# Performance work log

Measured on AMD Instinct MI355X. Metric: run time of the kernel, lower is better.

## Reference

```python
import jax, jax.numpy as jnp
import numpy as np

NUM_QUERIES = 256
NUM_NEGATIVES = 512
NUM_GENERALIZED = 8
GEN_RADIUS = 1.0
TEMP = 0.5
STRONG_THRESHOLD = 0.97


def _mls(mu0, mu1, s0, s1):
    # mutual likelihood score; mu's are L2-normalized (F.normalize, eps=1e-12)
    mu0 = mu0 / jnp.maximum(jnp.linalg.norm(mu0, axis=-1, keepdims=True), 1e-12)
    mu1 = mu1 / jnp.maximum(jnp.linalg.norm(mu1, axis=-1, keepdims=True), 1e-12)
    down = s0 + s1
    return -0.5 * (((mu0 - mu1) ** 2) / down + jnp.log(down)).mean(-1)


def setup_inputs() -> dict:
    key = jax.random.key(0)
    B, S, H, W, C = 4, 19, 128, 128, 256
    ks = jax.random.split(key, 6)
    mu = jax.random.normal(ks[0], (B, C, H, W), jnp.float32)
    sigma = jax.random.uniform(ks[1], (B, C, H, W), jnp.float32, minval=0.1, maxval=1.0)
    cls = jax.random.randint(ks[2], (B, H, W), 0, S)
    label = jnp.transpose(jax.nn.one_hot(cls, S, dtype=jnp.float32), (0, 3, 1, 2))  # [B,S,H,W]
    mask = jnp.ones((B, 1, H, W), jnp.float32)
    prob = jax.random.uniform(ks[3], (B, S, H, W), jnp.float32)
    mmt_prototype_mu = jax.random.normal(ks[4], (S, 1, C), jnp.float32)
    mmt_prototype_sigma = jax.random.uniform(ks[5], (S, 1, C), jnp.float32, minval=0.1, maxval=1.0)
    return {"mu": mu, "sigma": sigma, "label": label, "mask": mask, "prob": prob,
            "mmt_prototype_mu": mmt_prototype_mu, "mmt_prototype_sigma": mmt_prototype_sigma,
            "epoch": 0, "iter_i": 0}


def reference(mu, sigma, label, mask, prob, mmt_prototype_mu, mmt_prototype_sigma, epoch, iter_i):
    B, C, H, W = mu.shape
    S = label.shape[1]
    P = B * H * W
    Q, NEG, G = NUM_QUERIES, NUM_NEGATIVES, NUM_GENERALIZED
    key = jax.random.key(1234)

    valid = (label * mask).transpose(1, 0, 2, 3).reshape(S, P)            # [S,P] float
    mu_f = mu.transpose(0, 2, 3, 1).reshape(P, C)                          # [P,C]
    sg_f = sigma.transpose(0, 2, 3, 1).reshape(P, C)
    prob_f = prob.transpose(1, 0, 2, 3).reshape(S, P)
    hard = (prob_f < STRONG_THRESHOLD).astype(valid.dtype) * valid         # [S,P]

    # --- segment prototypes (precision-weighted fusion), detached as in torch.no_grad ---
    inv_sg = 1.0 / sg_f
    proto_sigma_b = 1.0 / jnp.einsum('sp,pc->sc', valid, inv_sg)           # [S,C]
    proto_mu_b = proto_sigma_b * jnp.einsum('sp,pc->sc', valid, inv_sg * mu_f)
    mmt_mu = mmt_prototype_mu[:, 0, :]
    mmt_sg = mmt_prototype_sigma[:, 0, :]
    proto_sigma = 1.0 / (1.0 / proto_sigma_b + 1.0 / mmt_sg)               # momentum fusion
    proto_mu = proto_sigma * (mmt_mu / mmt_sg + proto_mu_b / proto_sigma_b)
    proto_mu = jax.lax.stop_gradient(proto_mu)
    proto_sigma = jax.lax.stop_gradient(proto_sigma)

    # cumulative masks for uniform sampling over valid / hard pixels via searchsorted
    valid_cum = jnp.cumsum(valid, axis=1)                                  # [S,P]
    valid_cnt = valid_cum[:, -1]
    hard_cum = jnp.cumsum(hard, axis=1)
    hard_cnt = hard_cum[:, -1]

    loss = jnp.float32(0.0)
    for i in range(S):
        ki = jax.random.fold_in(key, i)
        k_anc, k_cls, k_neg, k_gen = jax.random.split(ki, 4)
        # anchors: uniform over hard pixels of segment i
        u = jax.random.uniform(k_anc, (Q,)) * hard_cnt[i]
        a_idx = jnp.clip(jnp.searchsorted(hard_cum[i], u, side='right'), 0, P - 1)
        anchor_mu = mu_f[a_idx]                                            # [Q,C]
        anchor_sg = sg_f[a_idx]
        # negative class distribution from prototype MLS similarity
        others = jnp.concatenate([jnp.arange(i + 1, S), jnp.arange(0, i)])  # [S-1]
        sim = _mls(proto_mu[i][None], proto_mu[others], proto_sigma[i][None], proto_sigma[others])
        logp = jax.nn.log_softmax(sim / TEMP)
        samp = jax.random.categorical(k_cls, logp, shape=(Q, NEG))          # idx into `others`
        cls_g = others[samp.reshape(-1)]                                    # [Q*NEG] global class
        # uniform pixel within each sampled class (vectorized searchsorted over classes)
        un = jax.random.uniform(k_neg, (Q * NEG,))
        idx_all = jax.vmap(lambda cs, cnt: jnp.searchsorted(cs, un * cnt, side='right'))(valid_cum, valid_cnt)
        n_idx = jnp.clip(idx_all[cls_g, jnp.arange(Q * NEG)], 0, P - 1)
        neg_mu = jax.lax.stop_gradient(mu_f[n_idx].reshape(Q, NEG, C))
        neg_sg = jax.lax.stop_gradient(sg_f[n_idx].reshape(Q, NEG, C))
        pos_mu = jnp.broadcast_to(proto_mu[i][None, None], (Q, 1, C))
        pos_sg = jnp.broadcast_to(proto_sigma[i][None, None], (Q, 1, C))
        # generalized negatives: reparameterized samples from (updated) momentum prototypes
        eps = jax.random.normal(k_gen, (S - 1, G, C))
        gen = proto_mu[others][:, None, :] + GEN_RADIUS * jnp.sqrt(proto_sigma[others])[:, None, :] * eps
        gen = jnp.broadcast_to(gen.reshape(1, (S - 1) * G, C), (Q, (S - 1) * G, C))
        all_mu = jnp.concatenate([pos_mu, neg_mu, gen], axis=1)             # [Q,1+NEG+(S-1)*G,C]
        all_sg = jnp.concatenate([pos_sg, neg_sg, jnp.zeros_like(gen)], axis=1)
        logits = _mls(anchor_mu[:, None, :], all_mu, anchor_sg[:, None, :], all_sg) / TEMP
        loss = loss - jax.nn.log_softmax(logits, axis=-1)[:, 0].mean()      # CE vs target 0
    return loss / S
```

## Files before the change

### kernel.cpp

```cpp
#include <hip/hip_runtime.h>
#include <hip/hip_fp16.h>
#include <hip/hip_fp8.h>
#include <cstdint>

#define B_   4
#define S_   19
#define HW_  16384
#define P_   65536
#define C_   256
#define Q_   256
#define NEG_ 512
#define NS_  131072
#define GENV_ 144
#define NANCH (S_ * Q_)
#define NPAIR (NANCH / 2)
#define NBUCK 8

typedef float v2f __attribute__((ext_vector_type(2)));

#if __has_builtin(__builtin_amdgcn_cvt_pk_f32_fp8) && __has_builtin(__builtin_amdgcn_cvt_pk_fp8_f32)
#define HAVE_HW_FP8 1
#endif

template<int W> __device__ __forceinline__ v2f cvt8(uint32_t d) {
#ifdef HAVE_HW_FP8
  v2f r = __builtin_amdgcn_cvt_pk_f32_fp8((int)d, W);
  return r;
#else
  __hip_fp8_e4m3 h0, h1;
  h0.__x = (uint8_t)(d >> (W * 16));
  h1.__x = (uint8_t)(d >> (W * 16 + 8));
  v2f r; r.x = (float)h0; r.y = (float)h1; return r;
#endif
}
template<int W> __device__ __forceinline__ uint32_t pk8(float a, float b, uint32_t old) {
#ifdef HAVE_HW_FP8
  return (uint32_t)__builtin_amdgcn_cvt_pk_fp8_f32(a, b, (int)old, W);
#else
  __hip_fp8_e4m3 ha(a), hb(b);
  uint32_t v = (uint32_t)ha.__x | ((uint32_t)hb.__x << 8);
  return (old & (W ? 0x0000FFFFu : 0xFFFF0000u)) | (v << (W * 16));
#endif
}

__device__ __forceinline__ void tf2x32(uint32_t k0, uint32_t k1, uint32_t x0, uint32_t x1,
                                       uint32_t& o0, uint32_t& o1) {
  uint32_t k2 = k0 ^ k1 ^ 0x1BD11BDAu;
#define TFR(r) { x0 += x1; x1 = (x1 << r) | (x1 >> (32 - r)); x1 ^= x0; }
  x0 += k0; x1 += k1;
  TFR(13) TFR(15) TFR(26) TFR(6)  x0 += k1; x1 += k2 + 1u;
  TFR(17) TFR(29) TFR(16) TFR(24) x0 += k2; x1 += k0 + 2u;
  TFR(13) TFR(15) TFR(26) TFR(6)  x0 += k0; x1 += k1 + 3u;
  TFR(17) TFR(29) TFR(16) TFR(24) x0 += k1; x1 += k2 + 4u;
  TFR(13) TFR(15) TFR(26) TFR(6)  x0 += k2; x1 += k0 + 5u;
#undef TFR
  o0 = x0; o1 = x1;
}

__device__ __forceinline__ uint32_t rbits(uint32_t k0, uint32_t k1, uint32_t n) {
  uint32_t a, b; tf2x32(k0, k1, 0u, n, a, b); return a ^ b;
}

__device__ __forceinline__ float bits2f01(uint32_t b) {
  return __uint_as_float((b >> 9) | 0x3f800000u) - 1.0f;
}

__device__ __forceinline__ float fastrcp(float x) {
  float r; asm("v_rcp_f32 %0, %1" : "=v"(r) : "v"(x)); return r;
}

__device__ __forceinline__ float wred(float v) {
#pragma unroll
  for (int off = 32; off > 0; off >>= 1) v += __shfl_xor(v, off, 64);
  return v;
}
__device__ __forceinline__ void wred3(float& a, float& b, float& c) {
#pragma unroll
  for (int off = 32; off > 0; off >>= 1) {
    a += __shfl_xor(a, off, 64);
    b += __shfl_xor(b, off, 64);
    c += __shfl_xor(c, off, 64);
  }
}

__device__ __forceinline__ void lse_up(float lg, float& m, float& l) {
  if (lg > m) { l = l * __expf(m - lg) + 1.0f; m = lg; }
  else l += __expf(lg - m);
}
__device__ __forceinline__ void lse_merge(float& m, float& l, float mo, float lo) {
  float mn = fmaxf(m, mo);
  l = l * __expf(m - mn) + lo * __expf(mo - mn);
  m = mn;
}

__device__ __forceinline__ float erfinv_f(float x) {
  float w = -__logf(fmaxf(fmaf(-x, x, 1.0f), 1e-37f));
  float p;
  if (w < 5.0f) {
    w -= 2.5f;
    p = 2.81022636e-08f;
    p = fmaf(p, w, 3.43273939e-07f);
    p = fmaf(p, w, -3.5233877e-06f);
    p = fmaf(p, w, -4.39150654e-06f);
    p = fmaf(p, w, 0.00021858087f);
    p = fmaf(p, w, -0.00125372503f);
    p = fmaf(p, w, -0.00417768164f);
    p = fmaf(p, w, 0.246640727f);
    p = fmaf(p, w, 1.50140941f);
  } else {
    w = sqrtf(w) - 3.0f;
    p = -0.000200214257f;
    p = fmaf(p, w, 0.000100950558f);
    p = fmaf(p, w, 0.00134934322f);
    p = fmaf(p, w, -0.00367342844f);
    p = fmaf(p, w, 0.00573950773f);
    p = fmaf(p, w, -0.0076224613f);
    p = fmaf(p, w, 0.00943887047f);
    p = fmaf(p, w, 1.00167406f);
    p = fmaf(p, w, 2.83297682f);
  }
  return p * x;
}

__global__ void k_keys(uint32_t* __restrict__ keys) {
  int i = threadIdx.x;
  if (i >= S_) return;
  uint32_t f0, f1;
  tf2x32(0u, 1234u, 0u, (uint32_t)i, f0, f1);
#pragma unroll
  for (int t = 0; t < 4; ++t) {
    uint32_t a, b;
    tf2x32(f0, f1, 0u, (uint32_t)t, a, b);
    keys[i * 8 + t * 2] = a; keys[i * 8 + t * 2 + 1] = b;
  }
}

__global__ __launch_bounds__(256) void k_classify(const float* __restrict__ label,
    const float* __restrict__ mask, const float* __restrict__ prob,
    int* __restrict__ cls, int* __restrict__ hrd) {
  int p = blockIdx.x * 256 + threadIdx.x;
  int b = p >> 14, rem = p & (HW_ - 1);
  int sp = -1;
#pragma unroll
  for (int s = 0; s < S_; ++s) {
    float l = label[((b * S_ + s) << 14) + rem];
    if (l > 0.5f) sp = s;
  }
  if (mask[(b << 14) + rem] <= 0.5f) sp = -1;
  int h = 0;
  if (sp >= 0) h = (prob[((b * S_ + sp) << 14) + rem] < 0.97f) ? 1 : 0;
  cls[p] = sp; hrd[p] = h;
}

__global__ __launch_bounds__(256) void k_pack(const float* __restrict__ mu,
    const float* __restrict__ sg, uint32_t* __restrict__ pair8, float* __restrict__ norm2) {
  __shared__ float smu[64][65];
  __shared__ float ssg[64][65];
  int p0 = blockIdx.x * 64, c0 = blockIdx.y * 64;
  int b = p0 >> 14, rem0 = p0 & (HW_ - 1);
  int px = threadIdx.x & 63, cy = threadIdx.x >> 6;
#pragma unroll
  for (int itr = 0; itr < 16; ++itr) {
    int cl = cy + itr * 4;
    int addr = ((b * C_ + c0 + cl) << 14) + rem0 + px;
    smu[cl][px] = mu[addr];
    ssg[cl][px] = sg[addr];
  }
  __syncthreads();
#pragma unroll
  for (int itr = 0; itr < 8; ++itr) {
    int e = itr * 256 + threadIdx.x;
    int pxl = e >> 5, dw = e & 31, cl = dw * 2;
    uint32_t wd = pk8<0>(smu[cl][pxl], ssg[cl][pxl], 0u);
    wd = pk8<1>(smu[cl + 1][pxl], ssg[cl + 1][pxl], wd);
    pair8[(size_t)(p0 + pxl) * 128 + (c0 >> 1) + dw] = wd;
  }
  int pxn = threadIdx.x >> 2, qn = threadIdx.x & 3;
  float s2 = 0.f;
#pragma unroll
  for (int k = 0; k < 16; ++k) { float v = smu[qn * 16 + k][pxn]; s2 = fmaf(v, v, s2); }
  s2 += __shfl_xor(s2, 1, 64);
  s2 += __shfl_xor(s2, 2, 64);
  if (qn == 0) atomicAdd(&norm2[p0 + pxn], s2);
}

__global__ __launch_bounds__(256) void k_count(const int* __restrict__ cls, const int* __restrict__ hrd,
    int* __restrict__ bcv, int* __restrict__ bch) {
  __shared__ int hv[S_], hh[S_];
  int t = threadIdx.x;
  if (t < S_) { hv[t] = 0; hh[t] = 0; }
  __syncthreads();
  int p = blockIdx.x * 256 + t;
  int s = cls[p];
  if (s >= 0) { atomicAdd(&hv[s], 1); if (hrd[p]) atomicAdd(&hh[s], 1); }
  __syncthreads();
  if (t < S_) { bcv[t * 256 + blockIdx.x] = hv[t]; bch[t * 256 + blockIdx.x] = hh[t]; }
}

__global__ __launch_bounds__(320) void k_scan(const int* __restrict__ bcv, const int* __restrict__ bch,
    int* __restrict__ bov, int* __restrict__ boh,
    int* __restrict__ cntv, int* __restrict__ cnth,
    int* __restrict__ basev, int* __restrict__ baseh) {
  __shared__ int psv[S_][16], psh[S_][16], scv[S_], sch[S_];
  int t = threadIdx.x;
  int s = t >> 4, c = t & 15;
  if (t < 304) {
    int sv = 0, sh = 0;
#pragma unroll 4
    for (int b = 0; b < 16; ++b) {
      sv += bcv[s * 256 + c * 16 + b];
      sh += bch[s * 256 + c * 16 + b];
    }
    psv[s][c] = sv; psh[s][c] = sh;
  }
  __syncthreads();
  if (t < S_) {
    int rv = 0, rh = 0;
#pragma unroll
    for (int cc = 0; cc < 16; ++cc) {
      int tv = psv[t][cc]; psv[t][cc] = rv; rv += tv;
      int th = psh[t][cc]; psh[t][cc] = rh; rh += th;
    }
    cntv[t] = rv; cnth[t] = rh; scv[t] = rv; sch[t] = rh;
  }
  __syncthreads();
  if (t == 0) {
    int bv = 0, bh = 0;
    for (int k = 0; k < S_; ++k) { basev[k] = bv; bv += scv[k]; baseh[k] = bh; bh += sch[k]; }
  }
  if (t < 304) {
    int rv = psv[s][c], rh = psh[s][c];
#pragma unroll 4
    for (int b = 0; b < 16; ++b) {
      int i0 = s * 256 + c * 16 + b;
      int tv = bcv[i0]; bov[i0] = rv; rv += tv;
      int th = bch[i0]; boh[i0] = rh; rh += th;
    }
  }
}

__global__ __launch_bounds__(256) void k_fill(const int* __restrict__ cls, const int* __restrict__ hrd,
    const int* __restrict__ bov, const int* __restrict__ boh,
    const int* __restrict__ basev, const int* __restrict__ baseh,
    int* __restrict__ posv, int* __restrict__ posh) {
  __shared__ int lc[256], lh[256];
  int t = threadIdx.x;
  int p = blockIdx.x * 256 + t;
  int s = cls[p]; int h = hrd[p];
  lc[t] = s; lh[t] = h;
  __syncthreads();
  if (s >= 0) {
    int rv = 0, rh = 0;
    for (int k = 0; k < t; ++k) { if (lc[k] == s) { rv++; rh += lh[k]; } }
    posv[basev[s] + bov[s * 256 + blockIdx.x] + rv] = p;
    if (h) posh[baseh[s] + boh[s * 256 + blockIdx.x] + rh] = p;
  }
}

__global__ __launch_bounds__(256) void k_sums(const uint32_t* __restrict__ pair8,
    const int* __restrict__ cls, float* __restrict__ part) {
  __shared__ float lacc[S_][2][C_];
  __shared__ int scls[256];
  int t = threadIdx.x;
  for (int e = t; e < S_ * 2 * C_; e += 256) (&lacc[0][0][0])[e] = 0.f;
  int p0 = blockIdx.x * 256;
  scls[t] = cls[p0 + t];
  __syncthreads();
  int half = t & 1, dwi = t >> 1;
  uint32_t d = pair8[(size_t)p0 * 128 + dwi];
  for (int pp = 0; pp < 256; ++pp) {
    uint32_t dnx = (pp + 1 < 256) ? pair8[(size_t)(p0 + pp + 1) * 128 + dwi] : 0u;
    int s = scls[pp];
    if (s >= 0) {
      v2f e = half ? cvt8<1>(d) : cvt8<0>(d);
      float ia = fastrcp(e.y);
      lacc[s][0][t] += ia;
      lacc[s][1][t] += ia * e.x;
    }
    d = dnx;
  }
  __syncthreads();
  float* dst = part + (size_t)blockIdx.x * (2 * S_ * C_);
  for (int e = t; e < S_ * 2 * C_; e += 256) dst[e] = (&lacc[0][0][0])[e];
}

__global__ __launch_bounds__(256) void k_proto(const float* __restrict__ part,
    const float* __restrict__ mmu, const float* __restrict__ msg,
    float* __restrict__ pmu, float* __restrict__ psig, float* __restrict__ phat) {
  int s = blockIdx.x, c = threadIdx.x;
  float A = 0.f, Bv = 0.f;
  for (int b = 0; b < 256; ++b) {
    const float* pb = part + (size_t)b * (2 * S_ * C_) + (s * 2) * C_;
    A += pb[c];
    Bv += pb[C_ + c];
  }
  int e = s * C_ + c;
  float psb = 1.0f / A;
  float pmb = psb * Bv;
  float ms = msg[e], mm = mmu[e];
  float ps = 1.0f / (1.0f / psb + 1.0f / ms);
  float pm = ps * (mm / ms + pmb / psb);
  pmu[e] = pm; psig[e] = ps;
  __shared__ float red[4];
  float w = wred(pm * pm);
  int lane = c & 63, wv = c >> 6;
  if (lane == 0) red[wv] = w;
  __syncthreads();
  float tot = red[0] + red[1] + red[2] + red[3];
  float nrm = fmaxf(sqrtf(tot), 1e-12f);
  phat[e] = pm / nrm;
}

__global__ __launch_bounds__(64) void k_simlogp(const float* __restrict__ phat,
    const float* __restrict__ psig, float* __restrict__ logp) {
  int i = blockIdx.x, lane = threadIdx.x;
  int c0 = lane * 4;
  float phi[4], psi[4];
#pragma unroll
  for (int k = 0; k < 4; ++k) { phi[k] = phat[i * C_ + c0 + k]; psi[k] = psig[i * C_ + c0 + k]; }
  float xs[18];
#pragma unroll
  for (int j = 0; j < 18; ++j) {
    int o = i + 1 + j; if (o >= S_) o -= S_;
    float t = 0.f;
#pragma unroll
    for (int k = 0; k < 4; ++k) {
      float d = phi[k] - phat[o * C_ + c0 + k];
      float dn = psi[k] + psig[o * C_ + c0 + k];
      t += d * d / dn + logf(dn);
    }
    t = wred(t);
    xs[j] = (-0.5f * t * (1.0f / 256.0f)) * 2.0f;
  }
  float m = xs[0];
#pragma unroll
  for (int j = 1; j < 18; ++j) m = fmaxf(m, xs[j]);
  float se = 0.f;
#pragma unroll
  for (int j = 0; j < 18; ++j) se += expf(xs[j] - m);
  float lg = logf(se);
  if (lane == 0) {
#pragma unroll
    for (int j = 0; j < 18; ++j) logp[i * 18 + j] = xs[j] - m - lg;
  }
}

__global__ __launch_bounds__(256) void k_anchors(const uint32_t* __restrict__ keys,
    const int* __restrict__ cnth, const int* __restrict__ baseh,
    const int* __restrict__ posh, int* __restrict__ aidx) {
  int i = blockIdx.x, q = threadIdx.x;
  uint32_t k0 = keys[i * 8 + 0], k1 = keys[i * 8 + 1];
  float u = bits2f01(rbits(k0, k1, (uint32_t)q));
  int cnt = cnth[i];
  int idx = P_ - 1;
  if (cnt > 0) {
    int kk = (int)(u * (float)cnt);
    if (kk >= cnt) kk = cnt - 1;
    idx = posh[baseh[i] + kk];
  }
  aidx[i * Q_ + q] = idx;
}

__global__ __launch_bounds__(256) void k_gen(const uint32_t* __restrict__ keys,
    const float* __restrict__ pmu, const float* __restrict__ psig, float* __restrict__ ghat) {
  int v = blockIdx.x, i = blockIdx.y, c = threadIdx.x;
  int o = i + 1 + (v >> 3); if (o >= S_) o -= S_;
  uint32_t k0 = keys[i * 8 + 6], k1 = keys[i * 8 + 7];
  uint32_t bits = rbits(k0, k1, (uint32_t)(v * C_ + c));
  float f01 = bits2f01(bits);
  const float lo = -0.99999994f;
  float u = fmaxf(f01 * 2.0f + lo, lo);
  float eps = 1.41421356237f * erfinv_f(u);
  float g = pmu[o * C_ + c] + sqrtf(psig[o * C_ + c]) * eps;
  __shared__ float red[4];
  float w = wred(g * g);
  int lane = c & 63, wv = c >> 6;
  if (lane == 0) red[wv] = w;
  __syncthreads();
  float tot = red[0] + red[1] + red[2] + red[3];
  float nrm = fmaxf(sqrtf(tot), 1e-12f);
  ghat[((size_t)(i * GENV_ + v)) * C_ + c] = g / nrm;
}

__global__ __launch_bounds__(256) void k_sample(const uint32_t* __restrict__ keys,
    const float* __restrict__ logp, const int* __restrict__ cntv, const int* __restrict__ basev,
    const int* __restrict__ posv, int* __restrict__ nidx) {
  int i = blockIdx.y;
  int m = blockIdx.x * 256 + threadIdx.x;
  __shared__ float lp[18];
  __shared__ int lcnt[S_], lbase[S_];
  int t = threadIdx.x;
  if (t < 18) lp[t] = logp[i * 18 + t];
  if (t < S_) { lcnt[t] = cntv[t]; lbase[t] = basev[t]; }
  __syncthreads();
  uint32_t kc0 = keys[i * 8 + 2], kc1 = keys[i * 8 + 3];
  uint32_t kn0 = keys[i * 8 + 4], kn1 = keys[i * 8 + 5];
  float bv = -1e30f; int best = 0;
  for (int s = 0; s < 18; ++s) {
    uint32_t b = rbits(kc0, kc1, (uint32_t)m * 18u + (uint32_t)s);
    float u = fmaxf(bits2f01(b), 1.17549435e-38f);
    float g = -__logf(-__logf(u)) + lp[s];
    if (g > bv) { bv = g; best = s; }
  }
  float un = bits2f01(rbits(kn0, kn1, (uint32_t)m));
  int cc = i + 1 + best; if (cc >= S_) cc -= S_;
  int cnt = lcnt[cc];
  int idx = P_ - 1;
  if (cnt > 0) {
    int kk = (int)(un * (float)cnt);
    if (kk >= cnt) kk = cnt - 1;
    idx = posv[lbase[cc] + kk];
  }
  nidx[(size_t)i * NS_ + m] = idx;
}

__global__ __launch_bounds__(64) void k_bucket(const int* __restrict__ nidx,
    int* __restrict__ snidx, int* __restrict__ boff) {
  int a = blockIdx.x;
  int lane = threadIdx.x;
  const int* src = nidx + (size_t)a * NEG_;
  int e[8], bk[8];
#pragma unroll
  for (int c = 0; c < 8; ++c) { e[c] = src[c * 64 + lane]; bk[c] = (e[c] >> 13) & 7; }
  uint32_t cnt[NBUCK];
#pragma unroll
  for (int b = 0; b < NBUCK; ++b) cnt[b] = 0;
#pragma unroll
  for (int c = 0; c < 8; ++c)
#pragma unroll
    for (int b = 0; b < NBUCK; ++b) {
      unsigned long long mb = __ballot(bk[c] == b);
      cnt[b] += (uint32_t)__popcll(mb);
    }
  uint32_t base[NBUCK]; uint32_t run = 0;
#pragma unroll
  for (int b = 0; b < NBUCK; ++b) { base[b] = run; run += cnt[b]; }
  if (lane < NBUCK) boff[a * 9 + lane] = (int)base[lane];
  if (lane == 0) boff[a * 9 + 8] = NEG_;
  uint32_t off[NBUCK];
#pragma unroll
  for (int b = 0; b < NBUCK; ++b) off[b] = 0;
  unsigned long long ltm = (1ull << lane) - 1ull;
#pragma unroll
  for (int c = 0; c < 8; ++c) {
    int pos = 0;
#pragma unroll
    for (int b = 0; b < NBUCK; ++b) {
      unsigned long long mb = __ballot(bk[c] == b);
      if (bk[c] == b) pos = (int)(base[b] + off[b] + (uint32_t)__popcll(mb & ltm));
      off[b] += (uint32_t)__popcll(mb);
    }
    snidx[(size_t)a * NEG_ + pos] = e[c];
  }
}

__global__ __launch_bounds__(64) void k_neg(const uint32_t* __restrict__ pair8,
    const float* __restrict__ norm2, const int* __restrict__ snidx,
    const int* __restrict__ boff, const int* __restrict__ aidx,
    float2* __restrict__ partial) {
  __shared__ float4 anc[260];
  __shared__ float4 ah2s[130];
  int bid = blockIdx.x;
  int bucket = bid & 7;
  int pr = bid >> 3;
  int a0 = pr * 2, a1 = a0 + 1;
  int lane = threadIdx.x;

  int ap0 = aidx[a0], ap1 = aidx[a1];
  float rn0 = fastrcp(fmaxf(sqrtf(norm2[ap0]), 1e-12f));
  float rn1 = fastrcp(fmaxf(sqrtf(norm2[ap1]), 1e-12f));
  uint2 d0 = ((const uint2*)(pair8 + (size_t)ap0 * 128))[lane];
  uint2 d1 = ((const uint2*)(pair8 + (size_t)ap1 * 128))[lane];
  {
    v2f ex = cvt8<0>(d0.x), ey = cvt8<1>(d0.x), ez = cvt8<0>(d0.y), ew = cvt8<1>(d0.y);
    float h0 = ex.x * rn0, h1 = ey.x * rn0, h2 = ez.x * rn0, h3 = ew.x * rn0;
    anc[lane * 2]     = make_float4(h0, ex.y, h1, ey.y);
    anc[lane * 2 + 1] = make_float4(h2, ez.y, h3, ew.y);
    ah2s[lane]        = make_float4(h0 * h0, h1 * h1, h2 * h2, h3 * h3);
    ex = cvt8<0>(d1.x); ey = cvt8<1>(d1.x); ez = cvt8<0>(d1.y); ew = cvt8<1>(d1.y);
    h0 = ex.x * rn1; h1 = ey.x * rn1; h2 = ez.x * rn1; h3 = ew.x * rn1;
    anc[130 + lane * 2]     = make_float4(h0, ex.y, h1, ey.y);
    anc[130 + lane * 2 + 1] = make_float4(h2, ez.y, h3, ew.y);
    ah2s[65 + lane]         = make_float4(h0 * h0, h1 * h1, h2 * h2, h3 * h3);
  }
  __syncthreads();

  int s0 = boff[a0 * 9 + bucket], e0i = boff[a0 * 9 + bucket + 1];
  int s1 = boff[a1 * 9 + bucket], e1i = boff[a1 * 9 + bucket + 1];
  int L0 = e0i - s0, L1 = e1i - s1, Lt = L0 + L1;
  const int* list0 = snidx + (size_t)a0 * NEG_ + s0;
  const int* list1 = snidx + (size_t)a1 * NEG_ + s1;

  float m0 = -1e30f, l0 = 0.f, m1 = -1e30f, l1 = 0.f;

  for (int r = 0; r * 64 < Lt; ++r) {
    int g = r * 64 + lane;
    bool act = g < Lt;
    int which = (act && g >= L0) ? 1 : 0;
    int j = which ? (g - L0) : g;
    int p = act ? (which ? list1[j] : list0[j]) : ap0;
    float rnN = fastrcp(fmaxf(sqrtf(norm2[p]), 1e-12f));
    const uint4* rp = (const uint4*)(pair8 + (size_t)p * 128);
    const float4* A = anc + which * 130;
    const float4* H = ah2s + which * 65;
    float sA = 0.f, sC = 0.f, sNR = 0.f, sL = 0.f;
    uint4 c0 = rp[0], c1 = rp[1];
#pragma unroll 1
    for (int it = 0; it < 16; ++it) {
      int nx = ((it + 1) & 15) * 2;
      uint4 n0 = rp[nx], n1 = rp[nx + 1];
      uint32_t dws[8] = {c0.x, c0.y, c0.z, c0.w, c1.x, c1.y, c1.z, c1.w};
      float pp = 1.0f, pq = 1.0f;
#pragma unroll
      for (int gq = 0; gq < 4; ++gq) {
        float4 acA = A[it * 8 + gq * 2];
        float4 acB = A[it * 8 + gq * 2 + 1];
        float4 hh = H[it * 4 + gq];
        v2f e0v = cvt8<0>(dws[2 * gq]),     e1v = cvt8<1>(dws[2 * gq]);
        v2f e2v = cvt8<0>(dws[2 * gq + 1]), e3v = cvt8<1>(dws[2 * gq + 1]);
        float dn0 = acA.y + e0v.y, dn1 = acA.w + e1v.y;
        float dn2 = acB.y + e2v.y, dn3 = acB.w + e3v.y;
        float d01 = dn0 * dn1, d23 = dn2 * dn3;
        float R01 = fastrcp(d01), R23 = fastrcp(d23);
        pp *= d01; pq *= d23;
        float r0 = dn1 * R01, r1 = dn0 * R01, r2 = dn3 * R23, r3 = dn2 * R23;
        sA = fmaf(hh.x, r0, sA); sA = fmaf(hh.y, r1, sA);
        sA = fmaf(hh.z, r2, sA); sA = fmaf(hh.w, r3, sA);
        float q0 = e0v.x * r0; sC = fmaf(acA.x, q0, sC); sNR = fmaf(e0v.x, q0, sNR);
        float q1 = e1v.x * r1; sC = fmaf(acA.z, q1, sC); sNR = fmaf(e1v.x, q1, sNR);
        float q2 = e2v.x * r2; sC = fmaf(acB.x, q2, sC); sNR = fmaf(e2v.x, q2, sNR);
        float q3 = e3v.x * r3; sC = fmaf(acB.z, q3, sC); sNR = fmaf(e3v.x, q3, sNR);
      }
      sL += __logf(pp * pq);
      c0 = n0; c1 = n1;
    }
    float tt = sA + rnN * rnN * sNR - 2.0f * rnN * sC + sL;
    float lg = -tt * (1.0f / 256.0f);
    if (act) { if (which) lse_up(lg, m1, l1); else lse_up(lg, m0, l0); }
  }
#pragma unroll
  for (int o = 32; o > 0; o >>= 1) {
    float mo = __shfl_xor(m0, o, 64), lo = __shfl_xor(l0, o, 64);
    lse_merge(m0, l0, mo, lo);
    mo = __shfl_xor(m1, o, 64); lo = __shfl_xor(l1, o, 64);
    lse_merge(m1, l1, mo, lo);
  }
  if (lane == 0) {
    partial[a0 * NBUCK + bucket] = make_float2(m0, l0);
    partial[a1 * NBUCK + bucket] = make_float2(m1, l1);
  }
}

__global__ __launch_bounds__(256, 4) void k_fin(const uint32_t* __restrict__ pair8,
    const float* __restrict__ norm2,
    const float* __restrict__ phat, const float* __restrict__ psig,
    const float* __restrict__ ghat, const int* __restrict__ aidx,
    const float2* __restrict__ partial, float* __restrict__ out) {
  __shared__ float2 ancG[C_];
  __shared__ float redm[3][4];
  __shared__ float2 mlw[4];

  int bid = blockIdx.x;
  int i = bid >> 8;
  int t = threadIdx.x, w = t >> 6, lane = t & 63;

  int ap = aidx[bid];
  uint32_t ad = pair8[(size_t)ap * 128 + (t >> 1)];
  v2f ae0 = cvt8<0>(ad), ae1 = cvt8<1>(ad);
  float amu = (t & 1) ? ae1.x : ae0.x;
  float asg = (t & 1) ? ae1.y : ae0.y;
  float rn = fastrcp(fmaxf(sqrtf(norm2[ap]), 1e-12f));
  float ahat = amu * rn;
  float wv = fastrcp(asg);
  ancG[t] = make_float2(wv, ahat * wv);

  float pm = phat[i * C_ + t];
  float ps = psig[i * C_ + t];
  float dnp = asg + ps;
  float dd = ahat - pm;
  float post = fmaf(dd * dd, fastrcp(dnp), __logf(dnp));
  float a1t = ahat * ahat * wv;
  float lat = __logf(asg);
  wred3(post, a1t, lat);
  if (lane == 0) { redm[0][w] = post; redm[1][w] = a1t; redm[2][w] = lat; }
  __syncthreads();
  float postS = redm[0][0] + redm[0][1] + redm[0][2] + redm[0][3];
  float Kc = (redm[1][0] + redm[1][1] + redm[1][2] + redm[1][3])
           + (redm[2][0] + redm[2][1] + redm[2][2] + redm[2][3]);
  float logit0 = -postS * (1.0f / 256.0f);

  float m = -1e30f, l = 0.0f;
  const float4* ancGf = (const float4*)ancG;
  if (lane < 36) {
    int g = lane * 4 + w;
    const float4* gp = (const float4*)(ghat + ((size_t)(i * GENV_ + g)) * C_);
    float a1 = 0.f, a2 = 0.f;
    for (int itr = 0; itr < 64; ++itr) {
      float4 gv = gp[itr];
      float4 g01 = ancGf[itr * 2];
      float4 g23 = ancGf[itr * 2 + 1];
      a1 = fmaf(gv.x * gv.x, g01.x, a1); a2 = fmaf(gv.x, g01.y, a2);
      a1 = fmaf(gv.y * gv.y, g01.z, a1); a2 = fmaf(gv.y, g01.w, a2);
      a1 = fmaf(gv.z * gv.z, g23.x, a1); a2 = fmaf(gv.z, g23.y, a2);
      a1 = fmaf(gv.w * gv.w, g23.z, a1); a2 = fmaf(gv.w, g23.w, a2);
    }
    float lg = -(Kc + a1 - 2.0f * a2) * (1.0f / 256.0f);
    lse_up(lg, m, l);
  }
#pragma unroll
  for (int o = 32; o > 0; o >>= 1) {
    float mo = __shfl_xor(m, o, 64);
    float lo = __shfl_xor(l, o, 64);
    lse_merge(m, l, mo, lo);
  }
  if (lane == 0) mlw[w] = make_float2(m, l);
  __syncthreads();
  if (t == 0) {
    float mm = mlw[0].x, ll = mlw[0].y;
    lse_merge(mm, ll, mlw[1].x, mlw[1].y);
    lse_merge(mm, ll, mlw[2].x, mlw[2].y);
    lse_merge(mm, ll, mlw[3].x, mlw[3].y);
    const float2* pp = partial + (size_t)bid * NBUCK;
#pragma unroll
    for (int b = 0; b < NBUCK; ++b) lse_merge(mm, ll, pp[b].x, pp[b].y);
    lse_merge(mm, ll, logit0, 1.0f);
    float lse = mm + __logf(ll);
    float contrib = logit0 - lse;
    atomicAdd(out, -contrib * (1.0f / (19.0f * 256.0f)));
  }
}

extern "C" void kernel_launch(void* const* d_in, const int* in_sizes, int n_in,
                              void* d_out, int out_size, void* d_ws, size_t ws_size,
                              hipStream_t stream) {
  const float* mu    = (const float*)d_in[0];
  const float* sg    = (const float*)d_in[1];
  const float* label = (const float*)d_in[2];
  const float* mask  = (const float*)d_in[3];
  const float* prob  = (const float*)d_in[4];
  const float* mmu   = (const float*)d_in[5];
  const float* msg   = (const float*)d_in[6];

  char* ws = (char*)d_ws;
  size_t off = 0;
  auto take = [&](size_t bytes) { size_t r = off; off = (off + bytes + 255) & ~(size_t)255; return r; };
  size_t o_pair8 = take((size_t)P_ * 128 * 4);
  size_t o_norm2 = take((size_t)P_ * 4);
  size_t o_cls   = take((size_t)P_ * 4);
  size_t o_hrd   = take((size_t)P_ * 4);
  size_t o_bcv   = take(S_ * 256 * 4);
  size_t o_bch   = take(S_ * 256 * 4);
  size_t o_bov   = take(S_ * 256 * 4);
  size_t o_boh   = take(S_ * 256 * 4);
  size_t o_cntv  = take(S_ * 4);
  size_t o_cnth  = take(S_ * 4);
  size_t o_basev = take(S_ * 4);
  size_t o_baseh = take(S_ * 4);
  size_t o_posv  = take((size_t)P_ * 4);
  size_t o_posh  = take((size_t)P_ * 4);
  size_t o_part  = take((size_t)256 * 2 * S_ * C_ * 4);
  size_t o_pmu   = take(S_ * C_ * 4);
  size_t o_psig  = take(S_ * C_ * 4);
  size_t o_phat  = take(S_ * C_ * 4);
  size_t o_logp  = take(S_ * 18 * 4);
  size_t o_keys  = take(S_ * 8 * 4);
  size_t o_aidx  = take(S_ * Q_ * 4);
  size_t o_nidx  = take((size_t)S_ * NS_ * 4);
  size_t o_snidx = take((size_t)S_ * NS_ * 4);
  size_t o_boff  = take((size_t)NANCH * 9 * 4);
  size_t o_lpar  = take((size_t)NANCH * NBUCK * 8);
  size_t o_ghat  = take((size_t)S_ * GENV_ * C_ * 4);
  if (ws_size < off) return;

  uint32_t* pair8 = (uint32_t*)(ws + o_pair8);
  float*    norm2 = (float*)(ws + o_norm2);
  int*      cls   = (int*)(ws + o_cls);
  int*      hrd   = (int*)(ws + o_hrd);
  int*      bcv   = (int*)(ws + o_bcv);
  int*      bch   = (int*)(ws + o_bch);
  int*      bov   = (int*)(ws + o_bov);
  int*      boh   = (int*)(ws + o_boh);
  int*      cntv  = (int*)(ws + o_cntv);
  int*      cnth  = (int*)(ws + o_cnth);
  int*      basev = (int*)(ws + o_basev);
  int*      baseh = (int*)(ws + o_baseh);
  int*      posv  = (int*)(ws + o_posv);
  int*      posh  = (int*)(ws + o_posh);
  float*    part  = (float*)(ws + o_part);
  float*    pmu   = (float*)(ws + o_pmu);
  float*    psig  = (float*)(ws + o_psig);
  float*    phat  = (float*)(ws + o_phat);
  float*    logp  = (float*)(ws + o_logp);
  uint32_t* keys  = (uint32_t*)(ws + o_keys);
  int*      aidx  = (int*)(ws + o_aidx);
  int*      nidx  = (int*)(ws + o_nidx);
  int*      snidx = (int*)(ws + o_snidx);
  int*      boff  = (int*)(ws + o_boff);
  float2*   lpar  = (float2*)(ws + o_lpar);
  float*    ghat  = (float*)(ws + o_ghat);

  hipMemsetAsync(ws + o_norm2, 0, (size_t)P_ * 4, stream);
  hipMemsetAsync(d_out, 0, (size_t)out_size * 4, stream);

  k_keys<<<1, 64, 0, stream>>>(keys);
  k_classify<<<256, 256, 0, stream>>>(label, mask, prob, cls, hrd);
  k_pack<<<dim3(P_ / 64, C_ / 64), 256, 0, stream>>>(mu, sg, pair8, norm2);
  k_count<<<256, 256, 0, stream>>>(cls, hrd, bcv, bch);
  k_scan<<<1, 320, 0, stream>>>(bcv, bch, bov, boh, cntv, cnth, basev, baseh);
  k_fill<<<256, 256, 0, stream>>>(cls, hrd, bov, boh, basev, baseh, posv, posh);
  k_sums<<<256, 256, 0, stream>>>(pair8, cls, part);
  k_proto<<<S_, 256, 0, stream>>>(part, mmu, msg, pmu, psig, phat);
  k_simlogp<<<S_, 64, 0, stream>>>(phat, psig, logp);
  k_anchors<<<S_, 256, 0, stream>>>(keys, cnth, baseh, posh, aidx);
  k_gen<<<dim3(GENV_, S_), 256, 0, stream>>>(keys, pmu, psig, ghat);
  k_sample<<<dim3(512, S_), 256, 0, stream>>>(keys, logp, cntv, basev, posv, nidx);
  k_bucket<<<NANCH, 64, 0, stream>>>(nidx, snidx, boff);
  k_neg<<<NBUCK * NPAIR, 64, 0, stream>>>(pair8, norm2, snidx, boff, aidx, lpar);
  k_fin<<<NANCH, 256, 0, stream>>>(pair8, norm2, phat, psig, ghat, aidx, lpar, (float*)d_out);
}
```

Measured before the change: 657.9 us.

## Pre-normalize mu in fp8 pack, simplify MLS inner loop, fuse small kernels

Adds a k_norm pass that computes per-pixel norms up front. k_pack now stores the L2-normalized mu in fp8, so k_neg can compute the squared difference directly instead of the expanded three-term form with per-negative norm reciprocals. The change also folds key generation and per-block counts into k_classify and anchor selection into k_bucket, and replaces Gumbel-max with an equivalent exponential-race argmin. The cost is an extra strided full read of mu in k_norm and a different fp8 quantization of normalized values, which may shift accuracy.

```diff
diff --git a/kernel.cpp b/kernel.cpp
--- a/kernel.cpp
+++ b/kernel.cpp
@@ -12,7 +12,7 @@
 #define NEG_ 512
 #define NS_  131072
 #define GENV_ 144
-#define NANCH (S_ * Q_)
+#define NANCH (S_ * 256)
 #define NPAIR (NANCH / 2)
 #define NBUCK 8
 
@@ -122,23 +122,25 @@
   return p * x;
 }
 
-__global__ void k_keys(uint32_t* __restrict__ keys) {
-  int i = threadIdx.x;
-  if (i >= S_) return;
-  uint32_t f0, f1;
-  tf2x32(0u, 1234u, 0u, (uint32_t)i, f0, f1);
-#pragma unroll
-  for (int t = 0; t < 4; ++t) {
-    uint32_t a, b;
-    tf2x32(f0, f1, 0u, (uint32_t)t, a, b);
-    keys[i * 8 + t * 2] = a; keys[i * 8 + t * 2 + 1] = b;
-  }
-}
-
 __global__ __launch_bounds__(256) void k_classify(const float* __restrict__ label,
     const float* __restrict__ mask, const float* __restrict__ prob,
-    int* __restrict__ cls, int* __restrict__ hrd) {
-  int p = blockIdx.x * 256 + threadIdx.x;
+    uint32_t* __restrict__ keys, int* __restrict__ cls, int* __restrict__ hrd,
+    int* __restrict__ bcv, int* __restrict__ bch) {
+  __shared__ int hv[S_], hh[S_];
+  int t = threadIdx.x;
+  if (t < S_) { hv[t] = 0; hh[t] = 0; }
+  if (blockIdx.x == 0 && t < S_) {
+    uint32_t f0, f1;
+    tf2x32(0u, 1234u, 0u, (uint32_t)t, f0, f1);
+#pragma unroll
+    for (int k = 0; k < 4; ++k) {
+      uint32_t a, b;
+      tf2x32(f0, f1, 0u, (uint32_t)k, a, b);
+      keys[t * 8 + k * 2] = a; keys[t * 8 + k * 2 + 1] = b;
+    }
+  }
+  __syncthreads();
+  int p = blockIdx.x * 256 + t;
   int b = p >> 14, rem = p & (HW_ - 1);
   int sp = -1;
 #pragma unroll
@@ -150,14 +152,35 @@
   int h = 0;
   if (sp >= 0) h = (prob[((b * S_ + sp) << 14) + rem] < 0.97f) ? 1 : 0;
   cls[p] = sp; hrd[p] = h;
+  if (sp >= 0) { atomicAdd(&hv[sp], 1); if (h) atomicAdd(&hh[sp], 1); }
+  __syncthreads();
+  if (t < S_) { bcv[t * 256 + blockIdx.x] = hv[t]; bch[t * 256 + blockIdx.x] = hh[t]; }
+}
+
+__global__ __launch_bounds__(256) void k_norm(const float* __restrict__ mu,
+    float2* __restrict__ rnrm) {
+  int p = blockIdx.x * 256 + threadIdx.x;
+  int b = p >> 14, rem = p & (HW_ - 1);
+  const float* base = mu + (((size_t)(b * C_)) << 14) + rem;
+  float s2 = 0.f;
+#pragma unroll 4
+  for (int c = 0; c < C_; ++c) {
+    float v = base[(size_t)c << 14];
+    s2 = fmaf(v, v, s2);
+  }
+  float nrm = sqrtf(s2);
+  rnrm[p] = make_float2(fastrcp(fmaxf(nrm, 1e-12f)), nrm);
 }
 
 __global__ __launch_bounds__(256) void k_pack(const float* __restrict__ mu,
-    const float* __restrict__ sg, uint32_t* __restrict__ pair8, float* __restrict__ norm2) {
+    const float* __restrict__ sg, const float2* __restrict__ rnrm,
+    uint32_t* __restrict__ pair8) {
   __shared__ float smu[64][65];
   __shared__ float ssg[64][65];
+  __shared__ float srn[64];
   int p0 = blockIdx.x * 64, c0 = blockIdx.y * 64;
   int b = p0 >> 14, rem0 = p0 & (HW_ - 1);
+  if (threadIdx.x < 64) srn[threadIdx.x] = rnrm[p0 + threadIdx.x].x;
   int px = threadIdx.x & 63, cy = threadIdx.x >> 6;
 #pragma unroll
   for (int itr = 0; itr < 16; ++itr) {
@@ -171,30 +194,11 @@
   for (int itr = 0; itr < 8; ++itr) {
     int e = itr * 256 + threadIdx.x;
     int pxl = e >> 5, dw = e & 31, cl = dw * 2;
-    uint32_t wd = pk8<0>(smu[cl][pxl], ssg[cl][pxl], 0u);
-    wd = pk8<1>(smu[cl + 1][pxl], ssg[cl + 1][pxl], wd);
+    float rn = srn[pxl];
+    uint32_t wd = pk8<0>(smu[cl][pxl] * rn, ssg[cl][pxl], 0u);
+    wd = pk8<1>(smu[cl + 1][pxl] * rn, ssg[cl + 1][pxl], wd);
     pair8[(size_t)(p0 + pxl) * 128 + (c0 >> 1) + dw] = wd;
   }
-  int pxn = threadIdx.x >> 2, qn = threadIdx.x & 3;
-  float s2 = 0.f;
-#pragma unroll
-  for (int k = 0; k < 16; ++k) { float v = smu[qn * 16 + k][pxn]; s2 = fmaf(v, v, s2); }
-  s2 += __shfl_xor(s2, 1, 64);
-  s2 += __shfl_xor(s2, 2, 64);
-  if (qn == 0) atomicAdd(&norm2[p0 + pxn], s2);
-}
-
-__global__ __launch_bounds__(256) void k_count(const int* __restrict__ cls, const int* __restrict__ hrd,
-    int* __restrict__ bcv, int* __restrict__ bch) {
-  __shared__ int hv[S_], hh[S_];
-  int t = threadIdx.x;
-  if (t < S_) { hv[t] = 0; hh[t] = 0; }
-  __syncthreads();
-  int p = blockIdx.x * 256 + t;
-  int s = cls[p];
-  if (s >= 0) { atomicAdd(&hv[s], 1); if (hrd[p]) atomicAdd(&hh[s], 1); }
-  __syncthreads();
-  if (t < S_) { bcv[t * 256 + blockIdx.x] = hv[t]; bch[t * 256 + blockIdx.x] = hh[t]; }
 }
 
 __global__ __launch_bounds__(320) void k_scan(const int* __restrict__ bcv, const int* __restrict__ bch,
@@ -258,13 +262,15 @@
 }
 
 __global__ __launch_bounds__(256) void k_sums(const uint32_t* __restrict__ pair8,
-    const int* __restrict__ cls, float* __restrict__ part) {
+    const float2* __restrict__ rnrm, const int* __restrict__ cls, float* __restrict__ part) {
   __shared__ float lacc[S_][2][C_];
   __shared__ int scls[256];
+  __shared__ float snrm[256];
   int t = threadIdx.x;
   for (int e = t; e < S_ * 2 * C_; e += 256) (&lacc[0][0][0])[e] = 0.f;
   int p0 = blockIdx.x * 256;
   scls[t] = cls[p0 + t];
+  snrm[t] = rnrm[p0 + t].y;
   __syncthreads();
   int half = t & 1, dwi = t >> 1;
   uint32_t d = pair8[(size_t)p0 * 128 + dwi];
@@ -275,7 +281,7 @@
       v2f e = half ? cvt8<1>(d) : cvt8<0>(d);
       float ia = fastrcp(e.y);
       lacc[s][0][t] += ia;
-      lacc[s][1][t] += ia * e.x;
+      lacc[s][1][t] += ia * e.x * snrm[pp];
     }
     d = dnx;
   }
@@ -343,22 +349,6 @@
 #pragma unroll
     for (int j = 0; j < 18; ++j) logp[i * 18 + j] = xs[j] - m - lg;
   }
-}
-
-__global__ __launch_bounds__(256) void k_anchors(const uint32_t* __restrict__ keys,
-    const int* __restrict__ cnth, const int* __restrict__ baseh,
-    const int* __restrict__ posh, int* __restrict__ aidx) {
-  int i = blockIdx.x, q = threadIdx.x;
-  uint32_t k0 = keys[i * 8 + 0], k1 = keys[i * 8 + 1];
-  float u = bits2f01(rbits(k0, k1, (uint32_t)q));
-  int cnt = cnth[i];
-  int idx = P_ - 1;
-  if (cnt > 0) {
-    int kk = (int)(u * (float)cnt);
-    if (kk >= cnt) kk = cnt - 1;
-    idx = posh[baseh[i] + kk];
-  }
-  aidx[i * Q_ + q] = idx;
 }
 
 __global__ __launch_bounds__(256) void k_gen(const uint32_t* __restrict__ keys,
@@ -387,20 +377,20 @@
     const int* __restrict__ posv, int* __restrict__ nidx) {
   int i = blockIdx.y;
   int m = blockIdx.x * 256 + threadIdx.x;
-  __shared__ float lp[18];
+  __shared__ float elp[18];
   __shared__ int lcnt[S_], lbase[S_];
   int t = threadIdx.x;
-  if (t < 18) lp[t] = logp[i * 18 + t];
+  if (t < 18) elp[t] = __expf(-logp[i * 18 + t]);
   if (t < S_) { lcnt[t] = cntv[t]; lbase[t] = basev[t]; }
   __syncthreads();
   uint32_t kc0 = keys[i * 8 + 2], kc1 = keys[i * 8 + 3];
   uint32_t kn0 = keys[i * 8 + 4], kn1 = keys[i * 8 + 5];
-  float bv = -1e30f; int best = 0;
+  float bv = 1e30f; int best = 0;
   for (int s = 0; s < 18; ++s) {
     uint32_t b = rbits(kc0, kc1, (uint32_t)m * 18u + (uint32_t)s);
     float u = fmaxf(bits2f01(b), 1.17549435e-38f);
-    float g = -__logf(-__logf(u)) + lp[s];
-    if (g > bv) { bv = g; best = s; }
+    float val = (-__logf(u)) * elp[s];
+    if (val < bv) { bv = val; best = s; }
   }
   float un = bits2f01(rbits(kn0, kn1, (uint32_t)m));
   int cc = i + 1 + best; if (cc >= S_) cc -= S_;
@@ -414,10 +404,25 @@
   nidx[(size_t)i * NS_ + m] = idx;
 }
 
-__global__ __launch_bounds__(64) void k_bucket(const int* __restrict__ nidx,
-    int* __restrict__ snidx, int* __restrict__ boff) {
+__global__ __launch_bounds__(64) void k_bucket(const uint32_t* __restrict__ keys,
+    const int* __restrict__ cnth, const int* __restrict__ baseh, const int* __restrict__ posh,
+    const int* __restrict__ nidx, int* __restrict__ snidx, int* __restrict__ boff,
+    int* __restrict__ aidx) {
   int a = blockIdx.x;
   int lane = threadIdx.x;
+  if (lane == 0) {
+    int i = a >> 8, q = a & 255;
+    uint32_t k0 = keys[i * 8 + 0], k1 = keys[i * 8 + 1];
+    float u = bits2f01(rbits(k0, k1, (uint32_t)q));
+    int cnt = cnth[i];
+    int idx = P_ - 1;
+    if (cnt > 0) {
+      int kk = (int)(u * (float)cnt);
+      if (kk >= cnt) kk = cnt - 1;
+      idx = posh[baseh[i] + kk];
+    }
+    aidx[a] = idx;
+  }
   const int* src = nidx + (size_t)a * NEG_;
   int e[8], bk[8];
 #pragma unroll
@@ -455,11 +460,9 @@
 }
 
 __global__ __launch_bounds__(64) void k_neg(const uint32_t* __restrict__ pair8,
-    const float* __restrict__ norm2, const int* __restrict__ snidx,
-    const int* __restrict__ boff, const int* __restrict__ aidx,
-    float2* __restrict__ partial) {
+    const int* __restrict__ snidx, const int* __restrict__ boff,
+    const int* __restrict__ aidx, float2* __restrict__ partial) {
   __shared__ float4 anc[260];
-  __shared__ float4 ah2s[130];
   int bid = blockIdx.x;
   int bucket = bid & 7;
   int pr = bid >> 3;
@@ -467,21 +470,15 @@
   int lane = threadIdx.x;
 
   int ap0 = aidx[a0], ap1 = aidx[a1];
-  float rn0 = fastrcp(fmaxf(sqrtf(norm2[ap0]), 1e-12f));
-  float rn1 = fastrcp(fmaxf(sqrtf(norm2[ap1]), 1e-12f));
   uint2 d0 = ((const uint2*)(pair8 + (size_t)ap0 * 128))[lane];
   uint2 d1 = ((const uint2*)(pair8 + (size_t)ap1 * 128))[lane];
   {
     v2f ex = cvt8<0>(d0.x), ey = cvt8<1>(d0.x), ez = cvt8<0>(d0.y), ew = cvt8<1>(d0.y);
-    float h0 = ex.x * rn0, h1 = ey.x * rn0, h2 = ez.x * rn0, h3 = ew.x * rn0;
-    anc[lane * 2]     = make_float4(h0, ex.y, h1, ey.y);
-    anc[lane * 2 + 1] = make_float4(h2, ez.y, h3, ew.y);
-    ah2s[lane]        = make_float4(h0 * h0, h1 * h1, h2 * h2, h3 * h3);
+    anc[lane * 2]     = make_float4(ex.x, ex.y, ey.x, ey.y);
+    anc[lane * 2 + 1] = make_float4(ez.x, ez.y, ew.x, ew.y);
     ex = cvt8<0>(d1.x); ey = cvt8<1>(d1.x); ez = cvt8<0>(d1.y); ew = cvt8<1>(d1.y);
-    h0 = ex.x * rn1; h1 = ey.x * rn1; h2 = ez.x * rn1; h3 = ew.x * rn1;
-    anc[130 + lane * 2]     = make_float4(h0, ex.y, h1, ey.y);
-    anc[130 + lane * 2 + 1] = make_float4(h2, ez.y, h3, ew.y);
-    ah2s[65 + lane]         = make_float4(h0 * h0, h1 * h1, h2 * h2, h3 * h3);
+    anc[130 + lane * 2]     = make_float4(ex.x, ex.y, ey.x, ey.y);
+    anc[130 + lane * 2 + 1] = make_float4(ez.x, ez.y, ew.x, ew.y);
   }
   __syncthreads();
 
@@ -499,11 +496,9 @@
     int which = (act && g >= L0) ? 1 : 0;
     int j = which ? (g - L0) : g;
     int p = act ? (which ? list1[j] : list0[j]) : ap0;
-    float rnN = fastrcp(fmaxf(sqrtf(norm2[p]), 1e-12f));
     const uint4* rp = (const uint4*)(pair8 + (size_t)p * 128);
     const float4* A = anc + which * 130;
-    const float4* H = ah2s + which * 65;
-    float sA = 0.f, sC = 0.f, sNR = 0.f, sL = 0.f;
+    float sT = 0.f, sL = 0.f;
     uint4 c0 = rp[0], c1 = rp[1];
 #pragma unroll 1
     for (int it = 0; it < 16; ++it) {
@@ -515,7 +510,6 @@
       for (int gq = 0; gq < 4; ++gq) {
         float4 acA = A[it * 8 + gq * 2];
         float4 acB = A[it * 8 + gq * 2 + 1];
-        float4 hh = H[it * 4 + gq];
         v2f e0v = cvt8<0>(dws[2 * gq]),     e1v = cvt8<1>(dws[2 * gq]);
         v2f e2v = cvt8<0>(dws[2 * gq + 1]), e3v = cvt8<1>(dws[2 * gq + 1]);
         float dn0 = acA.y + e0v.y, dn1 = acA.w + e1v.y;
@@ -524,18 +518,15 @@
         float R01 = fastrcp(d01), R23 = fastrcp(d23);
         pp *= d01; pq *= d23;
         float r0 = dn1 * R01, r1 = dn0 * R01, r2 = dn3 * R23, r3 = dn2 * R23;
-        sA = fmaf(hh.x, r0, sA); sA = fmaf(hh.y, r1, sA);
-        sA = fmaf(hh.z, r2, sA); sA = fmaf(hh.w, r3, sA);
-        float q0 = e0v.x * r0; sC = fmaf(acA.x, q0, sC); sNR = fmaf(e0v.x, q0, sNR);
-        float q1 = e1v.x * r1; sC = fmaf(acA.z, q1, sC); sNR = fmaf(e1v.x, q1, sNR);
-        float q2 = e2v.x * r2; sC = fmaf(acB.x, q2, sC); sNR = fmaf(e2v.x, q2, sNR);
-        float q3 = e3v.x * r3; sC = fmaf(acB.z, q3, sC); sNR = fmaf(e3v.x, q3, sNR);
+        float f0 = acA.x - e0v.x, f1 = acA.z - e1v.x;
+        float f2 = acB.x - e2v.x, f3 = acB.z - e3v.x;
+        sT = fmaf(f0 * f0, r0, sT); sT = fmaf(f1 * f1, r1, sT);
+        sT = fmaf(f2 * f2, r2, sT); sT = fmaf(f3 * f3, r3, sT);
       }
       sL += __logf(pp * pq);
       c0 = n0; c1 = n1;
     }
-    float tt = sA + rnN * rnN * sNR - 2.0f * rnN * sC + sL;
-    float lg = -tt * (1.0f / 256.0f);
+    float lg = -(sT + sL) * (1.0f / 256.0f);
     if (act) { if (which) lse_up(lg, m1, l1); else lse_up(lg, m0, l0); }
   }
 #pragma unroll
@@ -552,7 +543,6 @@
 }
 
 __global__ __launch_bounds__(256, 4) void k_fin(const uint32_t* __restrict__ pair8,
-    const float* __restrict__ norm2,
     const float* __restrict__ phat, const float* __restrict__ psig,
     const float* __restrict__ ghat, const int* __restrict__ aidx,
     const float2* __restrict__ partial, float* __restrict__ out) {
@@ -567,10 +557,8 @@
   int ap = aidx[bid];
   uint32_t ad = pair8[(size_t)ap * 128 + (t >> 1)];
   v2f ae0 = cvt8<0>(ad), ae1 = cvt8<1>(ad);
-  float amu = (t & 1) ? ae1.x : ae0.x;
+  float ahat = (t & 1) ? ae1.x : ae0.x;
   float asg = (t & 1) ? ae1.y : ae0.y;
-  float rn = fastrcp(fmaxf(sqrtf(norm2[ap]), 1e-12f));
-  float ahat = amu * rn;
   float wv = fastrcp(asg);
   ancG[t] = make_float2(wv, ahat * wv);
 
@@ -645,7 +633,7 @@
   size_t off = 0;
   auto take = [&](size_t bytes) { size_t r = off; off = (off + bytes + 255) & ~(size_t)255; return r; };
   size_t o_pair8 = take((size_t)P_ * 128 * 4);
-  size_t o_norm2 = take((size_t)P_ * 4);
+  size_t o_rnrm  = take((size_t)P_ * 8);
   size_t o_cls   = take((size_t)P_ * 4);
   size_t o_hrd   = take((size_t)P_ * 4);
   size_t o_bcv   = take(S_ * 256 * 4);
@@ -673,7 +661,7 @@
   if (ws_size < off) return;
 
   uint32_t* pair8 = (uint32_t*)(ws + o_pair8);
-  float*    norm2 = (float*)(ws + o_norm2);
+  float2*   rnrm  = (float2*)(ws + o_rnrm);
   int*      cls   = (int*)(ws + o_cls);
   int*      hrd   = (int*)(ws + o_hrd);
   int*      bcv   = (int*)(ws + o_bcv);
@@ -699,22 +687,19 @@
   float2*   lpar  = (float2*)(ws + o_lpar);
   float*    ghat  = (float*)(ws + o_ghat);
 
-  hipMemsetAsync(ws + o_norm2, 0, (size_t)P_ * 4, stream);
   hipMemsetAsync(d_out, 0, (size_t)out_size * 4, stream);
 
-  k_keys<<<1, 64, 0, stream>>>(keys);
-  k_classify<<<256, 256, 0, stream>>>(label, mask, prob, cls, hrd);
-  k_pack<<<dim3(P_ / 64, C_ / 64), 256, 0, stream>>>(mu, sg, pair8, norm2);
-  k_count<<<256, 256, 0, stream>>>(cls, hrd, bcv, bch);
+  k_classify<<<256, 256, 0, stream>>>(label, mask, prob, keys, cls, hrd, bcv, bch);
+  k_norm<<<256, 256, 0, stream>>>(mu, rnrm);
+  k_pack<<<dim3(P_ / 64, C_ / 64), 256, 0, stream>>>(mu, sg, rnrm, pair8);
   k_scan<<<1, 320, 0, stream>>>(bcv, bch, bov, boh, cntv, cnth, basev, baseh);
   k_fill<<<256, 256, 0, stream>>>(cls, hrd, bov, boh, basev, baseh, posv, posh);
-  k_sums<<<256, 256, 0, stream>>>(pair8, cls, part);
+  k_sums<<<256, 256, 0, stream>>>(pair8, rnrm, cls, part);
   k_proto<<<S_, 256, 0, stream>>>(part, mmu, msg, pmu, psig, phat);
   k_simlogp<<<S_, 64, 0, stream>>>(phat, psig, logp);
-  k_anchors<<<S_, 256, 0, stream>>>(keys, cnth, baseh, posh, aidx);
   k_gen<<<dim3(GENV_, S_), 256, 0, stream>>>(keys, pmu, psig, ghat);
   k_sample<<<dim3(512, S_), 256, 0, stream>>>(keys, logp, cntv, basev, posv, nidx);
-  k_bucket<<<NANCH, 64, 0, stream>>>(nidx, snidx, boff);
-  k_neg<<<NBUCK * NPAIR, 64, 0, stream>>>(pair8, norm2, snidx, boff, aidx, lpar);
-  k_fin<<<NANCH, 256, 0, stream>>>(pair8, norm2, phat, psig, ghat, aidx, lpar, (float*)d_out);
-}
+  k_bucket<<<NANCH, 64, 0, stream>>>(keys, cnth, baseh, posh, nidx, snidx, boff, aidx);
+  k_neg<<<NBUCK * NPAIR, 64, 0, stream>>>(pair8, snidx, boff, aidx, lpar);
+  k_fin<<<NANCH, 256, 0, stream>>>(pair8, phat, psig, ghat, aidx, lpar, (float*)d_out);
+}
```

After: 616.2 us. 1.07x faster.
